# Optimization experiments

Measured on AMD Instinct MI355X. Metric: run time of the kernel, lower is better.

Reference implementation:

```python
import jax, jax.numpy as jnp
import numpy as np

H = 1.0 / 257.0  # grid spacing (init arg h)
N = 258          # grid size including 1-cell Dirichlet halo


def _step(u, f, h):
    # 7-point (6-neighbor) stencil: conv3d with the fixed 3x3x3 kernel
    # having ones at the 6 face-adjacent positions, expressed as shifted slices.
    nb = (u[..., :-2, 1:-1, 1:-1] + u[..., 2:, 1:-1, 1:-1]
          + u[..., 1:-1, :-2, 1:-1] + u[..., 1:-1, 2:, 1:-1]
          + u[..., 1:-1, 1:-1, :-2] + u[..., 1:-1, 1:-1, 2:])
    return (nb + (h * h) * f[..., 1:-1, 1:-1, 1:-1]) / 6.0


def _hard_encode(w):
    # zero-Dirichlet pad by 1 on each spatial face (gd=0.0)
    return jnp.pad(w, ((0, 0), (0, 0), (1, 1), (1, 1), (1, 1)))


def setup_inputs() -> dict:
    key = jax.random.key(0)
    k1, k2 = jax.random.split(key)
    pre = jax.random.normal(k1, (1, 1, N, N, N), dtype=jnp.float32)
    f = jax.random.normal(k2, (1, 1, N, N, N), dtype=jnp.float32)
    return {"pre": pre, "f": f, "max_iter": 20}


def reference(pre, f, max_iter):
    w0 = _step(pre, f, H)  # first sweep uses pre directly (no re-pad)

    def body(i, w):
        return _step(_hard_encode(w), f, H)

    # remaining max_iter-1 sweeps; output shape [B,1,N-2,N-2,N-2]
    return jax.lax.fori_loop(1, max_iter, body, w0)
```

## Files before the change

### kernel.cpp

```cpp
#include <hip/hip_runtime.h>


#define NP 258
#define NI 256
#define HHC ((1.0f / 257.0f) * (1.0f / 257.0f))
#define SIXTH (1.0f / 6.0f)

#define TX 32
#define TY 32
#define CZ 16

#define SU_ROWS 36
#define SU_Q 10
#define SU_P 11
#define SW_ROWS 34
#define SW_Q 10
#define SW_P 11

__device__ __forceinline__ float4 ld4u(const float* p) {
    float4 v; __builtin_memcpy(&v, p, sizeof(float4)); return v;
}
__device__ __forceinline__ float4 zero4() { return make_float4(0.f, 0.f, 0.f, 0.f); }

__global__ void step_first_v(const float* __restrict__ pre,
                             const float* __restrict__ f,
                             float* __restrict__ out,
                             float* __restrict__ g) {
    const int tx = threadIdx.x;
    const int y  = blockIdx.y * 4 + threadIdx.y;
    const int z  = blockIdx.z;
    const int gx0 = 4 * tx;
    const size_t sP = (size_t)NP * NP;
    const size_t prow = (size_t)(z + 1) * sP + (size_t)(y + 1) * NP + 1;

    const float4 C  = ld4u(&pre[prow + gx0]);
    const float4 up = ld4u(&pre[prow - NP + gx0]);
    const float4 dn = ld4u(&pre[prow + NP + gx0]);
    const float4 zm = ld4u(&pre[prow - sP + gx0]);
    const float4 zp = ld4u(&pre[prow + sP + gx0]);
    float4 fv = ld4u(&f[prow + gx0]);
    fv.x *= HHC; fv.y *= HHC; fv.z *= HHC; fv.w *= HHC;

    float lft = __shfl_up(C.w, 1);
    if (tx == 0)  lft = pre[prow + gx0 - 1];
    float rgt = __shfl_down(C.x, 1);
    if (tx == 63) rgt = pre[prow + gx0 + 4];

    float4 o;
    o.x = (lft + C.y + up.x + dn.x + zm.x + zp.x + fv.x) * SIXTH;
    o.y = (C.x + C.z + up.y + dn.y + zm.y + zp.y + fv.y) * SIXTH;
    o.z = (C.y + C.w + up.z + dn.z + zm.z + zp.z + fv.z) * SIXTH;
    o.w = (C.z + rgt + up.w + dn.w + zm.w + zp.w + fv.w) * SIXTH;

    const size_t oi = ((size_t)z * NI + y) * NI + gx0;
    *reinterpret_cast<float4*>(&out[oi]) = o;
    *reinterpret_cast<float4*>(&g[oi])  = fv;
}

__global__ void step_last_v(const float4* __restrict__ u4,
                            const float4* __restrict__ g4,
                            float4* __restrict__ out4) {
    const int tx = threadIdx.x;
    const int y  = blockIdx.y * 4 + threadIdx.y;
    const int z  = blockIdx.z;
    const int rowq   = NI / 4;
    const int planeq = NI * rowq;
    const int r = z * planeq + y * rowq + tx;

    const float4 v = u4[r];
    float left  = __shfl_up(v.w, 1);
    float right = __shfl_down(v.x, 1);
    if (tx == 0)  left  = 0.0f;
    if (tx == 63) right = 0.0f;

    float4 nb;
    nb.x = left + v.y;
    nb.y = v.x  + v.z;
    nb.z = v.y  + v.w;
    nb.w = v.z  + right;

    if (y > 0)      { float4 b = u4[r - rowq];   nb.x += b.x; nb.y += b.y; nb.z += b.z; nb.w += b.w; }
    if (y < NI - 1) { float4 b = u4[r + rowq];   nb.x += b.x; nb.y += b.y; nb.z += b.z; nb.w += b.w; }
    if (z > 0)      { float4 b = u4[r - planeq]; nb.x += b.x; nb.y += b.y; nb.z += b.z; nb.w += b.w; }
    if (z < NI - 1) { float4 b = u4[r + planeq]; nb.x += b.x; nb.y += b.y; nb.z += b.z; nb.w += b.w; }

    const float4 gv = g4[r];
    float4 o;
    o.x = (nb.x + gv.x) * SIXTH;
    o.y = (nb.y + gv.y) * SIXTH;
    o.z = (nb.z + gv.z) * SIXTH;
    o.w = (nb.w + gv.w) * SIXTH;
    out4[r] = o;
}

__global__ __launch_bounds__(512, 8)
void step_fused2p(const float* __restrict__ u,
                  const float* __restrict__ g,
                  float* __restrict__ out) {
    __shared__ float4 su[3][SU_ROWS][SU_P];
    __shared__ float4 sw[3][SW_ROWS][SW_P];

    const int tid = threadIdx.x;

    const int lid = blockIdx.x + (blockIdx.y << 3) + (blockIdx.z << 6);
    const int swz = (lid & 7) * 128 + (lid >> 3);
    const int x0 = (swz & 7) * TX;
    const int y0 = ((swz >> 3) & 7) * TY;
    const int z0 = (swz >> 6) * CZ;
    const int zend = z0 + CZ;
    const int plq = NI * NI;

    const int lr = tid / SU_Q, lc = tid - lr * SU_Q;
    const bool lact = tid < SU_ROWS * SU_Q;
    const int lgy = y0 - 2 + lr, lgx0 = x0 - 4 + 4 * lc;
    const bool lxy = lact && lgy >= 0 && lgy < NI && lgx0 >= 0 && lgx0 < NI;
    const int lbase = lgy * NI + lgx0;

    const int wr = tid / SW_Q, wc = tid - wr * SW_Q;
    const bool wact = tid < SW_ROWS * SW_Q;
    const int wgy = y0 - 1 + wr, wgx0 = x0 - 4 + 4 * wc;
    const bool wxy = wact && wgy >= 0 && wgy < NI && wgx0 >= 0 && wgx0 < NI;
    const int wcm = (wc > 0) ? wc - 1 : 0;
    const int wcp = (wc < SU_Q - 1) ? wc + 1 : SU_Q - 1;
    const int wbase = wgy * NI + wgx0;

    const int orr = tid >> 3, oc = tid & 7;
    const bool oact = tid < 256;
    const int ogy = y0 + orr, ogx0 = x0 + 4 * oc;
    const int obase = ogy * NI + ogx0;

    float4 ru = zero4(), gwn = zero4(), gon = zero4();
    {
        const int pl = z0 - 2;
        if (lxy && pl >= 0)
            ru = *reinterpret_cast<const float4*>(&u[(size_t)pl * plq + lbase]);
    }

    for (int t = z0 - 4; t < zend; ++t) {
        if (lact) su[(t + 5) % 3][lr][lc] = ru;
        ru = zero4();
        {   const int pl = t + 3;
            if (t < zend - 1 && pl >= 0 && pl < NI && lxy)
                ru = *reinterpret_cast<const float4*>(&u[(size_t)pl * plq + lbase]);
        }
        const float4 gw = gwn;
        {   const int p2 = t + 2;
            if (t >= z0 - 3 && t < zend - 1 && p2 >= 0 && p2 < NI && wxy)
                gwn = *reinterpret_cast<const float4*>(&g[(size_t)p2 * plq + wbase]);
        }
        const float4 go = gon;
        {   const int p1 = t + 1;
            if (p1 >= z0 && p1 < zend && oact)
                gon = *reinterpret_cast<const float4*>(&g[(size_t)p1 * plq + obase]);
        }
        __syncthreads();
        if (wact && t >= z0 - 2) {
            const int pw = t + 1;
            float4 wv = zero4();
            if (wxy && pw >= 0 && pw < NI) {
                const int sc = (pw + 3) % 3, sm = (pw + 2) % 3, sp = (pw + 4) % 3;
                const float4 cc  = su[sc][wr + 1][wc];
                const float4 cp  = su[sc][wr + 1][wcm];
                const float4 cn  = su[sc][wr + 1][wcp];
                const float4 uy  = su[sc][wr][wc];
                const float4 dy  = su[sc][wr + 2][wc];
                const float4 zmv = su[sm][wr + 1][wc];
                const float4 zpv = su[sp][wr + 1][wc];
                wv.x = (cp.w + cc.y + uy.x + dy.x + zmv.x + zpv.x + gw.x) * SIXTH;
                wv.y = (cc.x + cc.z + uy.y + dy.y + zmv.y + zpv.y + gw.y) * SIXTH;
                wv.z = (cc.y + cc.w + uy.z + dy.z + zmv.z + zpv.z + gw.z) * SIXTH;
                wv.w = (cc.z + cn.x + uy.w + dy.w + zmv.w + zpv.w + gw.w) * SIXTH;
            }
            sw[(pw + 3) % 3][wr][wc] = wv;
        }
        __syncthreads();
        if (oact && t >= z0) {
            const int sc = (t + 3) % 3, sm = (t + 2) % 3, sp = (t + 4) % 3;
            const float4 cc  = sw[sc][orr + 1][oc + 1];
            const float4 cp  = sw[sc][orr + 1][oc];
            const float4 cn  = sw[sc][orr + 1][oc + 2];
            const float4 uy  = sw[sc][orr][oc + 1];
            const float4 dy  = sw[sc][orr + 2][oc + 1];
            const float4 zmv = sw[sm][orr + 1][oc + 1];
            const float4 zpv = sw[sp][orr + 1][oc + 1];
            float4 ov;
            ov.x = (cp.w + cc.y + uy.x + dy.x + zmv.x + zpv.x + go.x) * SIXTH;
            ov.y = (cc.x + cc.z + uy.y + dy.y + zmv.y + zpv.y + go.y) * SIXTH;
            ov.z = (cc.y + cc.w + uy.z + dy.z + zmv.z + zpv.z + go.z) * SIXTH;
            ov.w = (cc.z + cn.x + uy.w + dy.w + zmv.w + zpv.w + go.w) * SIXTH;
            *reinterpret_cast<float4*>(&out[(size_t)t * plq + obase]) = ov;
        }
    }
}

extern "C" void kernel_launch(void* const* d_in, const int* in_sizes, int n_in,
                              void* d_out, int out_size, void* d_ws, size_t ws_size,
                              hipStream_t stream) {
    const float* pre = (const float*)d_in[0];
    const float* f   = (const float*)d_in[1];
    float* out = (float*)d_out;
    float* buf = (float*)d_ws;
    const size_t nInt = (size_t)NI * NI * NI;
    float* g = buf + nInt;

    step_first_v<<<dim3(1, NI / 4, NI), dim3(64, 4, 1), 0, stream>>>(pre, f, out, g);

    float* cur = out;
    float* nxt = buf;
    dim3 fg(NI / TX, NI / TY, NI / CZ);
    for (int i = 0; i < 9; ++i) {
        step_fused2p<<<fg, dim3(512, 1, 1), 0, stream>>>(cur, g, nxt);
        float* tmp = cur; cur = nxt; nxt = tmp;
    }
    step_last_v<<<dim3(1, NI / 4, NI), dim3(64, 4, 1), 0, stream>>>(
        (const float4*)cur, (const float4*)g, (float4*)out);
}
```

Baseline: 451.1 us.

## Keep z-neighbors in registers and use one barrier per plane in fused stencil

Restructures the two-sweep fused stencil kernel so each thread keeps its own column's z-1/z/z+1 values in registers instead of reading them from a 3-plane shared ring. Shared memory now holds only 2 planes per stage. X neighbors come from wavefront shuffles, with shared reads only at tile and wave edges. The per-plane synchronisation drops from two barriers to one, and the output thread mapping is merged with the intermediate mapping, loading g directly. This cuts LDS traffic and barrier stalls. In exchange, the u reload per column adds global loads, more registers are used, and launch bounds drop to 4 waves per SIMD.

Result: slower. 568.1 us (+25.9%).

```diff
diff --git a/kernel.cpp b/kernel.cpp
--- a/kernel.cpp
+++ b/kernel.cpp
@@ -10,17 +10,13 @@
 #define TY 32
 #define CZ 16
 
-#define SU_ROWS 36
-#define SU_Q 10
-#define SU_P 11
-#define SW_ROWS 34
-#define SW_Q 10
-#define SW_P 11
-
 __device__ __forceinline__ float4 ld4u(const float* p) {
     float4 v; __builtin_memcpy(&v, p, sizeof(float4)); return v;
 }
 __device__ __forceinline__ float4 zero4() { return make_float4(0.f, 0.f, 0.f, 0.f); }
+__device__ __forceinline__ float4 ldg4(const float* p) {
+    return *reinterpret_cast<const float4*>(p);
+}
 
 __global__ void step_first_v(const float* __restrict__ pre,
                              const float* __restrict__ f,
@@ -93,103 +89,112 @@
     out4[r] = o;
 }
 
-__global__ __launch_bounds__(512, 8)
-void step_fused2p(const float* __restrict__ u,
+__global__ __launch_bounds__(512, 4)
+void step_fused2r(const float* __restrict__ u,
                   const float* __restrict__ g,
                   float* __restrict__ out) {
-    __shared__ float4 su[3][SU_ROWS][SU_P];
-    __shared__ float4 sw[3][SW_ROWS][SW_P];
+    __shared__ float4 su[2][36][13];
+    __shared__ float4 sw[2][34][11];
 
     const int tid = threadIdx.x;
 
     const int lid = blockIdx.x + (blockIdx.y << 3) + (blockIdx.z << 6);
-    const int swz = (lid & 7) * 128 + (lid >> 3);
-    const int x0 = (swz & 7) * TX;
-    const int y0 = ((swz >> 3) & 7) * TY;
-    const int z0 = (swz >> 6) * CZ;
+    const int swzid = (lid & 7) * 128 + (lid >> 3);
+    const int x0 = (swzid & 7) * TX;
+    const int y0 = ((swzid >> 3) & 7) * TY;
+    const int z0 = (swzid >> 6) * CZ;
     const int zend = z0 + CZ;
     const int plq = NI * NI;
 
-    const int lr = tid / SU_Q, lc = tid - lr * SU_Q;
-    const bool lact = tid < SU_ROWS * SU_Q;
-    const int lgy = y0 - 2 + lr, lgx0 = x0 - 4 + 4 * lc;
+    const int lr = tid / 12, lc = tid - lr * 12;
+    const bool lact = tid < 432;
+    const int lgy = y0 - 2 + lr, lgx0 = x0 - 8 + 4 * lc;
     const bool lxy = lact && lgy >= 0 && lgy < NI && lgx0 >= 0 && lgx0 < NI;
     const int lbase = lgy * NI + lgx0;
 
-    const int wr = tid / SW_Q, wc = tid - wr * SW_Q;
-    const bool wact = tid < SW_ROWS * SW_Q;
+    const int wr = tid / 10, wc = tid - wr * 10;
+    const bool wact = tid < 340;
     const int wgy = y0 - 1 + wr, wgx0 = x0 - 4 + 4 * wc;
     const bool wxy = wact && wgy >= 0 && wgy < NI && wgx0 >= 0 && wgx0 < NI;
-    const int wcm = (wc > 0) ? wc - 1 : 0;
-    const int wcp = (wc < SU_Q - 1) ? wc + 1 : SU_Q - 1;
     const int wbase = wgy * NI + wgx0;
 
-    const int orr = tid >> 3, oc = tid & 7;
-    const bool oact = tid < 256;
-    const int ogy = y0 + orr, ogx0 = x0 + 4 * oc;
-    const int obase = ogy * NI + ogx0;
-
-    float4 ru = zero4(), gwn = zero4(), gon = zero4();
+    const bool oact = wact && wr >= 1 && wr <= 32 && wc >= 1 && wc <= 8;
+    const int obase = (y0 + wr - 1) * NI + (x0 + 4 * (wc - 1));
+
+    float4 u_c = zero4(), u_zp = zero4(), ucn = zero4(), ru = zero4();
+    float4 w_zm = zero4(), w_c = zero4(), w_zp = zero4();
+    float4 gwn = zero4();
+
     {
-        const int pl = z0 - 2;
-        if (lxy && pl >= 0)
-            ru = *reinterpret_cast<const float4*>(&u[(size_t)pl * plq + lbase]);
+        const int pl = z0 - 1;
+        if (lxy && pl >= 0) ru = ldg4(&u[(size_t)pl * plq + lbase]);
+        if (wxy) {
+            if (z0 - 2 >= 0) u_zp = ldg4(&u[(size_t)(z0 - 2) * plq + wbase]);
+            if (z0 - 1 >= 0) ucn  = ldg4(&u[(size_t)(z0 - 1) * plq + wbase]);
+        }
     }
 
-    for (int t = z0 - 4; t < zend; ++t) {
-        if (lact) su[(t + 5) % 3][lr][lc] = ru;
+    for (int t = z0 - 3; t < zend; ++t) {
+        if (lact) su[(t + 2) & 1][lr][lc] = ru;
         ru = zero4();
-        {   const int pl = t + 3;
-            if (t < zend - 1 && pl >= 0 && pl < NI && lxy)
-                ru = *reinterpret_cast<const float4*>(&u[(size_t)pl * plq + lbase]);
+        {
+            const int pl = t + 3;
+            if (t < zend - 1 && pl < NI && lxy)
+                ru = ldg4(&u[(size_t)pl * plq + lbase]);
+        }
+        const float4 u_zm = u_c;
+        u_c = u_zp; u_zp = ucn;
+        ucn = zero4();
+        {
+            const int pl = t + 3;
+            if (t < zend - 1 && pl < NI && wxy)
+                ucn = ldg4(&u[(size_t)pl * plq + wbase]);
         }
         const float4 gw = gwn;
-        {   const int p2 = t + 2;
-            if (t >= z0 - 3 && t < zend - 1 && p2 >= 0 && p2 < NI && wxy)
-                gwn = *reinterpret_cast<const float4*>(&g[(size_t)p2 * plq + wbase]);
-        }
-        const float4 go = gon;
-        {   const int p1 = t + 1;
-            if (p1 >= z0 && p1 < zend && oact)
-                gon = *reinterpret_cast<const float4*>(&g[(size_t)p1 * plq + obase]);
+        gwn = zero4();
+        {
+            const int p2 = t + 2;
+            if (t < zend - 1 && p2 >= 0 && p2 < NI && wxy)
+                gwn = ldg4(&g[(size_t)p2 * plq + wbase]);
+        }
+
+        const float scpw = __shfl_up(u_c.w, 1);
+        const float scnx = __shfl_down(u_c.x, 1);
+        float4 wv = zero4();
+        const int pw = t + 1;
+        if (wact && t >= z0 - 2 && wxy && pw >= 0 && pw < NI) {
+            const int s = pw & 1;
+            const float4 uy = su[s][wr][wc + 1];
+            const float4 dy = su[s][wr + 2][wc + 1];
+            float lft = scpw, rgt = scnx;
+            if (wc == 0 || (tid & 63) == 0)  lft = su[s][wr + 1][wc].w;
+            if (wc == 9 || (tid & 63) == 63) rgt = su[s][wr + 1][wc + 2].x;
+            wv.x = (lft   + u_c.y + uy.x + dy.x + u_zm.x + u_zp.x + gw.x) * SIXTH;
+            wv.y = (u_c.x + u_c.z + uy.y + dy.y + u_zm.y + u_zp.y + gw.y) * SIXTH;
+            wv.z = (u_c.y + u_c.w + uy.z + dy.z + u_zm.z + u_zp.z + gw.z) * SIXTH;
+            wv.w = (u_c.z + rgt   + uy.w + dy.w + u_zm.w + u_zp.w + gw.w) * SIXTH;
+        }
+        w_zm = w_c; w_c = w_zp; w_zp = wv;
+        if (wact) sw[pw & 1][wr][wc] = wv;
+
+        const float ocpw = __shfl_up(w_c.w, 1);
+        const float ocnx = __shfl_down(w_c.x, 1);
+        if (oact && t >= z0) {
+            const int s = t & 1;
+            const float4 uy = sw[s][wr - 1][wc];
+            const float4 dy = sw[s][wr + 1][wc];
+            float lft = ocpw, rgt = ocnx;
+            if ((tid & 63) == 0)  lft = sw[s][wr][wc - 1].w;
+            if ((tid & 63) == 63) rgt = sw[s][wr][wc + 1].x;
+            const float4 go = ldg4(&g[(size_t)t * plq + obase]);
+            float4 ov;
+            ov.x = (lft   + w_c.y + uy.x + dy.x + w_zm.x + w_zp.x + go.x) * SIXTH;
+            ov.y = (w_c.x + w_c.z + uy.y + dy.y + w_zm.y + w_zp.y + go.y) * SIXTH;
+            ov.z = (w_c.y + w_c.w + uy.z + dy.z + w_zm.z + w_zp.z + go.z) * SIXTH;
+            ov.w = (w_c.z + rgt   + uy.w + dy.w + w_zm.w + w_zp.w + go.w) * SIXTH;
+            *reinterpret_cast<float4*>(&out[(size_t)t * plq + obase]) = ov;
         }
         __syncthreads();
-        if (wact && t >= z0 - 2) {
-            const int pw = t + 1;
-            float4 wv = zero4();
-            if (wxy && pw >= 0 && pw < NI) {
-                const int sc = (pw + 3) % 3, sm = (pw + 2) % 3, sp = (pw + 4) % 3;
-                const float4 cc  = su[sc][wr + 1][wc];
-                const float4 cp  = su[sc][wr + 1][wcm];
-                const float4 cn  = su[sc][wr + 1][wcp];
-                const float4 uy  = su[sc][wr][wc];
-                const float4 dy  = su[sc][wr + 2][wc];
-                const float4 zmv = su[sm][wr + 1][wc];
-                const float4 zpv = su[sp][wr + 1][wc];
-                wv.x = (cp.w + cc.y + uy.x + dy.x + zmv.x + zpv.x + gw.x) * SIXTH;
-                wv.y = (cc.x + cc.z + uy.y + dy.y + zmv.y + zpv.y + gw.y) * SIXTH;
-                wv.z = (cc.y + cc.w + uy.z + dy.z + zmv.z + zpv.z + gw.z) * SIXTH;
-                wv.w = (cc.z + cn.x + uy.w + dy.w + zmv.w + zpv.w + gw.w) * SIXTH;
-            }
-            sw[(pw + 3) % 3][wr][wc] = wv;
-        }
-        __syncthreads();
-        if (oact && t >= z0) {
-            const int sc = (t + 3) % 3, sm = (t + 2) % 3, sp = (t + 4) % 3;
-            const float4 cc  = sw[sc][orr + 1][oc + 1];
-            const float4 cp  = sw[sc][orr + 1][oc];
-            const float4 cn  = sw[sc][orr + 1][oc + 2];
-            const float4 uy  = sw[sc][orr][oc + 1];
-            const float4 dy  = sw[sc][orr + 2][oc + 1];
-            const float4 zmv = sw[sm][orr + 1][oc + 1];
-            const float4 zpv = sw[sp][orr + 1][oc + 1];
-            float4 ov;
-            ov.x = (cp.w + cc.y + uy.x + dy.x + zmv.x + zpv.x + go.x) * SIXTH;
-            ov.y = (cc.x + cc.z + uy.y + dy.y + zmv.y + zpv.y + go.y) * SIXTH;
-            ov.z = (cc.y + cc.w + uy.z + dy.z + zmv.z + zpv.z + go.z) * SIXTH;
-            ov.w = (cc.z + cn.x + uy.w + dy.w + zmv.w + zpv.w + go.w) * SIXTH;
-            *reinterpret_cast<float4*>(&out[(size_t)t * plq + obase]) = ov;
-        }
     }
 }
 
@@ -209,7 +214,7 @@
     float* nxt = buf;
     dim3 fg(NI / TX, NI / TY, NI / CZ);
     for (int i = 0; i < 9; ++i) {
-        step_fused2p<<<fg, dim3(512, 1, 1), 0, stream>>>(cur, g, nxt);
+        step_fused2r<<<fg, dim3(512, 1, 1), 0, stream>>>(cur, g, nxt);
         float* tmp = cur; cur = nxt; nxt = tmp;
     }
     step_last_v<<<dim3(1, NI / 4, NI), dim3(64, 4, 1), 0, stream>>>(
```
